# Kernel tuning notes

Measured on AMD Instinct MI355X. Metric: run time of the kernel, lower is better.

Reference implementation:

```python
import jax, jax.numpy as jnp
import numpy as np

V, F, H, P, C = 50000, 300, 256, 128, 10   # vocab, emb dim, n_hid, n_penultimate, n_class
B, S, N = 128, 16, 64                      # docs, sentences/doc, word nodes/sentence (last = master)
G, T = B * S, B * S * N                    # sentence graphs, total word nodes
EPS = 1e-5


def _mp(h, adj, w1, b1, w2, b2):
    # MessagePassing: neighborhood aggregation (block-diag spmm) + 2-layer ReLU MLP
    m = jnp.einsum('gij,gjf->gif', adj, h)
    return jax.nn.relu(jax.nn.relu(m @ w1 + b1) @ w2 + b2)


def _att(h, w, b, v, use_master):
    # Attention readout: alpha = softmax(relu(hW+b)v) over nodes, weighted sum;
    # with master node, last node is split off and concatenated to the pooled vector.
    if use_master:
        t, h = h[:, -1, :], h[:, :-1, :]
    logits = jnp.einsum('gnh,h->gn', jax.nn.relu(h @ w + b), v)
    alpha = jax.nn.softmax(logits, axis=1)
    pooled = jnp.einsum('gn,gnh->gh', alpha, h)
    return jnp.concatenate([pooled, t], axis=1) if use_master else pooled


def setup_inputs():
    key = jax.random.key(0)
    ks = iter(jax.random.split(key, 40))
    def nrm(shape, s=0.05):
        return jax.random.normal(next(ks), shape, jnp.float32) * s
    x = jax.random.randint(next(ks), (T,), 0, V)
    adj = jax.random.uniform(next(ks), (G, N, N), jnp.float32)
    adj = adj / jnp.sum(adj, -1, keepdims=True)         # row-normalized word-graph blocks
    adj_s = jax.random.uniform(next(ks), (B, S, S), jnp.float32)
    adj_s = adj_s / jnp.sum(adj_s, -1, keepdims=True)   # sentence-graph blocks (unused in sentence_att branch)
    return dict(
        x=x, adj=adj, adj_s=adj_s, shape0=N, shape1=S,
        emb=nrm((V, F), 0.1),
        mp0_w1=nrm((F, H)), mp0_b1=jnp.zeros((H,)), mp0_w2=nrm((H, H)), mp0_b2=jnp.zeros((H,)),
        mp1_w1=nrm((H, H)), mp1_b1=jnp.zeros((H,)), mp1_w2=nrm((H, H)), mp1_b2=jnp.zeros((H,)),
        att0_w=nrm((H, H)), att0_b=jnp.zeros((H,)), att0_v=nrm((H,)),
        att1_w=nrm((H, H)), att1_b=jnp.zeros((H,)), att1_v=nrm((H,)),
        bn_gamma=jnp.ones((4 * H,)), bn_beta=jnp.zeros((4 * H,)),
        fc1_w=nrm((4 * H, H)), fc1_b=jnp.zeros((H,)),
        satt_w=nrm((H, H)), satt_b=jnp.zeros((H,)), satt_v=nrm((H,)),
        fc2_w=nrm((H, P)), fc2_b=jnp.zeros((P,)),
        fc3_w=nrm((P, C)), fc3_b=jnp.zeros((C,)),
    )


def reference(x, adj, adj_s, shape0, shape1, emb,
              mp0_w1, mp0_b1, mp0_w2, mp0_b2,
              mp1_w1, mp1_b1, mp1_w2, mp1_b2,
              att0_w, att0_b, att0_v, att1_w, att1_b, att1_v,
              bn_gamma, bn_beta, fc1_w, fc1_b,
              satt_w, satt_b, satt_v, fc2_w, fc2_b, fc3_w, fc3_b):
    h = emb[x].reshape(-1, shape0, emb.shape[1])        # [G, N, F] (dropout is identity at eval)
    reps = []
    for (w1, b1, w2, b2, aw, ab, av) in (
            (mp0_w1, mp0_b1, mp0_w2, mp0_b2, att0_w, att0_b, att0_v),
            (mp1_w1, mp1_b1, mp1_w2, mp1_b2, att1_w, att1_b, att1_v)):
        h = _mp(h, adj, w1, b1, w2, b2)                  # [G, N, H]
        reps.append(_att(h, aw, ab, av, True))           # [G, 2H]
    z = jnp.concatenate(reps, axis=1)                    # [G, 2*n_mp*H] = [G, 4H]
    mu, var = jnp.mean(z, 0), jnp.var(z, 0)              # BatchNorm1d (batch statistics)
    z = (z - mu) / jnp.sqrt(var + EPS) * bn_gamma + bn_beta
    z = jax.nn.relu(z @ fc1_w + fc1_b)                   # [G, H]
    z = z.reshape(-1, shape1, z.shape[1])                # [B, S, H]
    z = _att(z, satt_w, satt_b, satt_v, False)           # sentence attention -> [B, H]
    z = jax.nn.relu(z @ fc2_w + fc2_b)                   # [B, P]
    z = z @ fc3_w + fc3_b                                # [B, C]
    return jax.nn.log_softmax(z, axis=1)
```

## Files before the change

### kernel.cpp

```cpp
#include <hip/hip_runtime.h>
#include <math.h>


typedef unsigned short u16;
typedef __attribute__((ext_vector_type(8))) short bf16x8;
typedef __attribute__((ext_vector_type(4))) float f32x4;

__device__ __forceinline__ float b2f(u16 v){ return __uint_as_float(((unsigned)v)<<16); }
__device__ __forceinline__ u16 f2b(float f){
    unsigned u = __float_as_uint(f);
    return (u16)((u + 0x7FFFu + ((u>>16)&1u)) >> 16);
}
__device__ __forceinline__ ushort4 pack4(float a,float b,float c,float d){
    ushort4 o; o.x=f2b(a); o.y=f2b(b); o.z=f2b(c); o.w=f2b(d); return o;
}

#define SCOL_OFF 32768
__device__ __forceinline__ int srow_b(int nd, int f){
    return (nd*512 + f*2) ^ ((nd&7)<<4);
}
__device__ __forceinline__ int scol_b(int f, int nd){
    return SCOL_OFF + ((f*128 + nd*2) ^ ((f&7)<<4));
}
__device__ __forceinline__ int wfrag_off(int ni){
    return ((ni>>1)<<10) + ((ni&1)<<9);
}

__global__ __attribute__((amdgpu_flat_work_group_size(512,512),
                          amdgpu_waves_per_eu(1,2)))
void mega_k(
    const int* __restrict__ x, const u16* __restrict__ adjb,
    const u16* __restrict__ eprime,
    const u16* __restrict__ wb_w2a, const u16* __restrict__ wb_awa,
    const u16* __restrict__ wb_w1b, const u16* __restrict__ wb_w2b,
    const u16* __restrict__ wb_awb,
    const float* __restrict__ b1a, const float* __restrict__ b2a,
    const float* __restrict__ aba, const float* __restrict__ ava,
    const float* __restrict__ b1b, const float* __restrict__ b2b,
    const float* __restrict__ abb, const float* __restrict__ avb,
    u16* __restrict__ zb)
{
    __shared__ __align__(16) char sm[131072];
    const int tid = threadIdx.x;
    const int w = tid>>6, l = tid&63, lgp = l>>4, ll = l&15;
    const int q = w>>2, w4 = w&3, slab = w4*64;
    const long g = (long)blockIdx.x*2 + q;
    char* smq = sm + q*65536;
    const f32x4 zero4 = {0.f,0.f,0.f,0.f};

    {
        const int r2 = tid >> 3;
        const int fc = (tid & 7) * 32;
        #pragma unroll
        for (int q2=0; q2<2; ++q2){
            const u16* ep = eprime + (long)x[((long)blockIdx.x*2+q2)*64 + r2]*256 + fc;
            char* smr = sm + q2*65536;
            uint4 qa = *(const uint4*)(ep);
            uint4 qb = *(const uint4*)(ep + 8);
            uint4 qc = *(const uint4*)(ep + 16);
            uint4 qd = *(const uint4*)(ep + 24);
            #pragma unroll
            for (int qi=0; qi<4; ++qi){
                uint4 v = (qi==0)?qa:(qi==1)?qb:(qi==2)?qc:qd;
                unsigned xw[4] = {v.x, v.y, v.z, v.w};
                #pragma unroll
                for (int wi=0; wi<4; ++wi){
                    unsigned u = xw[wi];
                    int f0 = fc + qi*8 + wi*2;
                    *(u16*)(smr + scol_b(f0,   r2)) = (u16)(u & 0xffffu);
                    *(u16*)(smr + scol_b(f0+1, r2)) = (u16)(u >> 16);
                }
            }
        }
        __syncthreads();
    }

    const u16* adjg = adjb + g*4096;

    #pragma unroll 1
    for (int layer=0; layer<2; ++layer){
        const u16* wb_w2 = layer ? wb_w2b : wb_w2a;
        const u16* wb_aw = layer ? wb_awb : wb_awa;
        const float* b1  = layer ? b1b : b1a;
        const float* b2  = layer ? b2b : b2a;
        const float* ab  = layer ? abb : aba;
        const float* av  = layer ? avb : ava;
        const int zoff   = layer ? 512 : 0;

        {
            f32x4 acc[4][4];
            #pragma unroll
            for (int i=0;i<4;++i){
                #pragma unroll
                for (int j=0;j<4;++j) acc[i][j] = zero4;
            }
            #pragma unroll
            for (int t=0;t<2;++t){
                const int k0 = t*32 + lgp*8;
                bf16x8 a[4], b[4];
                #pragma unroll
                for (int mi=0;mi<4;++mi)
                    a[mi] = *(const bf16x8*)(smq + scol_b(slab + mi*16 + ll, k0));
                #pragma unroll
                for (int ni=0;ni<4;++ni)
                    b[ni] = *(const bf16x8*)(adjg + (ni*16+ll)*64 + k0);
                #pragma unroll
                for (int mi=0;mi<4;++mi){
                    #pragma unroll
                    for (int ni=0;ni<4;++ni)
                        acc[mi][ni] = __builtin_amdgcn_mfma_f32_16x16x32_bf16(a[mi], b[ni], acc[mi][ni],0,0,0);
                }
            }
            #pragma unroll
            for (int mi=0;mi<4;++mi){
                int f0 = slab + mi*16 + lgp*4;
                float4 bi = *(const float4*)(b1 + f0);
                #pragma unroll
                for (int ni=0;ni<4;++ni){
                    int nd = ni*16 + ll;
                    f32x4 v = acc[mi][ni];
                    *(ushort4*)(smq + srow_b(nd, f0)) = pack4(
                        fmaxf(v[0]+bi.x,0.f), fmaxf(v[1]+bi.y,0.f),
                        fmaxf(v[2]+bi.z,0.f), fmaxf(v[3]+bi.w,0.f));
                }
            }
            __syncthreads();
        }

        {
            f32x4 acc[4][4];
            #pragma unroll
            for (int i=0;i<4;++i){
                #pragma unroll
                for (int j=0;j<4;++j) acc[i][j] = zero4;
            }
            const u16* chw = wb_w2 + ((w4*2)<<10) + ll*32 + lgp*8;
            #pragma unroll
            for (int t=0;t<8;++t){
                const u16* ct = chw + t*8192;
                const int k0 = t*32 + lgp*8;
                bf16x8 cw0 = *(const bf16x8*)(ct + wfrag_off(0));
                bf16x8 cw1 = *(const bf16x8*)(ct + wfrag_off(1));
                bf16x8 cw2 = *(const bf16x8*)(ct + wfrag_off(2));
                bf16x8 cw3 = *(const bf16x8*)(ct + wfrag_off(3));
                bf16x8 b[4];
                #pragma unroll
                for (int ni=0;ni<4;++ni) b[ni] = *(const bf16x8*)(smq + srow_b(ni*16+ll, k0));
                #pragma unroll
                for (int ni=0;ni<4;++ni){
                    acc[0][ni] = __builtin_amdgcn_mfma_f32_16x16x32_bf16(cw0, b[ni], acc[0][ni],0,0,0);
                    acc[1][ni] = __builtin_amdgcn_mfma_f32_16x16x32_bf16(cw1, b[ni], acc[1][ni],0,0,0);
                    acc[2][ni] = __builtin_amdgcn_mfma_f32_16x16x32_bf16(cw2, b[ni], acc[2][ni],0,0,0);
                    acc[3][ni] = __builtin_amdgcn_mfma_f32_16x16x32_bf16(cw3, b[ni], acc[3][ni],0,0,0);
                }
            }
            __syncthreads();
            #pragma unroll
            for (int mi=0;mi<4;++mi){
                int f0 = slab + mi*16 + lgp*4;
                float4 bi = *(const float4*)(b2 + f0);
                #pragma unroll
                for (int ni=0;ni<4;++ni){
                    int nd = ni*16 + ll;
                    f32x4 v = acc[mi][ni];
                    *(ushort4*)(smq + srow_b(nd, f0)) = pack4(
                        fmaxf(v[0]+bi.x,0.f), fmaxf(v[1]+bi.y,0.f),
                        fmaxf(v[2]+bi.z,0.f), fmaxf(v[3]+bi.w,0.f));
                }
            }
            __syncthreads();
        }

        {
            f32x4 acc[4][4];
            #pragma unroll
            for (int i=0;i<4;++i){
                #pragma unroll
                for (int j=0;j<4;++j) acc[i][j] = zero4;
            }
            const u16* chw = wb_aw + ((w4*2)<<10) + ll*32 + lgp*8;
            #pragma unroll
            for (int t=0;t<8;++t){
                const u16* ct = chw + t*8192;
                const int k0 = t*32 + lgp*8;
                bf16x8 cw0 = *(const bf16x8*)(ct + wfrag_off(0));
                bf16x8 cw1 = *(const bf16x8*)(ct + wfrag_off(1));
                bf16x8 cw2 = *(const bf16x8*)(ct + wfrag_off(2));
                bf16x8 cw3 = *(const bf16x8*)(ct + wfrag_off(3));
                bf16x8 a[4];
                #pragma unroll
                for (int mi=0;mi<4;++mi) a[mi] = *(const bf16x8*)(smq + srow_b(mi*16+ll, k0));
                #pragma unroll
                for (int mi=0;mi<4;++mi){
                    acc[mi][0] = __builtin_amdgcn_mfma_f32_16x16x32_bf16(a[mi], cw0, acc[mi][0],0,0,0);
                    acc[mi][1] = __builtin_amdgcn_mfma_f32_16x16x32_bf16(a[mi], cw1, acc[mi][1],0,0,0);
                    acc[mi][2] = __builtin_amdgcn_mfma_f32_16x16x32_bf16(a[mi], cw2, acc[mi][2],0,0,0);
                    acc[mi][3] = __builtin_amdgcn_mfma_f32_16x16x32_bf16(a[mi], cw3, acc[mi][3],0,0,0);
                }
            }
            float abv[4], avv[4];
            #pragma unroll
            for (int ni=0;ni<4;++ni){
                int c = slab + ni*16 + ll;
                abv[ni] = ab[c]; avv[ni] = av[c];
            }
            float lgt[4][4];
            #pragma unroll
            for (int mi=0;mi<4;++mi){
                #pragma unroll
                for (int r=0;r<4;++r) lgt[mi][r] = 0.f;
            }
            #pragma unroll
            for (int mi=0;mi<4;++mi){
                #pragma unroll
                for (int ni=0;ni<4;++ni){
                    f32x4 v = acc[mi][ni];
                    #pragma unroll
                    for (int r=0;r<4;++r) lgt[mi][r] += fmaxf(v[r]+abv[ni],0.f)*avv[ni];
                }
            }
            #pragma unroll
            for (int mi=0;mi<4;++mi){
                #pragma unroll
                for (int r=0;r<4;++r){
                    float vv = lgt[mi][r];
                    vv += __shfl_xor(vv,1,64); vv += __shfl_xor(vv,2,64);
                    vv += __shfl_xor(vv,4,64); vv += __shfl_xor(vv,8,64);
                    lgt[mi][r] = vv;
                }
            }
            float* red = (float*)(smq + SCOL_OFF);
            if (ll == 0){
                #pragma unroll
                for (int mi=0;mi<4;++mi){
                    #pragma unroll
                    for (int r=0;r<4;++r){
                        int node = mi*16 + lgp*4 + r;
                        red[w4*64 + node] = lgt[mi][r];
                    }
                }
            }
            __syncthreads();
            if (tid < 128){
                int qs = tid >> 6, t64 = tid & 63;
                const float* rq = (const float*)(sm + qs*65536 + SCOL_OFF);
                float lv = rq[t64] + rq[64+t64] + rq[128+t64] + rq[192+t64];
                float v = (t64 < 63) ? lv : -INFINITY;
                float m = v;
                #pragma unroll
                for (int off=32; off; off>>=1) m = fmaxf(m, __shfl_xor(m, off, 64));
                float e = (t64 < 63) ? expf(v - m) : 0.f;
                float s = e;
                #pragma unroll
                for (int off=32; off; off>>=1) s += __shfl_xor(s, off, 64);
                *(float*)(sm + qs*65536 + SCOL_OFF + 1024 + t64*4) = e / s;
            }
            __syncthreads();
            {
                int qs = tid >> 8, c = tid & 255;
                char* smr = sm + qs*65536;
                const float* alpha = (const float*)(smr + SCOL_OFF + 1024);
                float pool = 0.f;
                for (int r=0;r<63;++r)
                    pool += alpha[r]*b2f(*(const u16*)(smr + srow_b(r,c)));
                long zb0 = ((long)blockIdx.x*2 + qs)*1024 + zoff;
                zb[zb0 + c]       = f2b(pool);
                zb[zb0 + 256 + c] = *(const u16*)(smr + srow_b(63,c));
            }
            __syncthreads();
        }

        if (layer == 0){
            f32x4 acc[4][4];
            #pragma unroll
            for (int i=0;i<4;++i){
                #pragma unroll
                for (int j=0;j<4;++j) acc[i][j] = zero4;
            }
            const u16* chw = wb_w1b + ((w4*2)<<10) + ll*32 + lgp*8;
            #pragma unroll
            for (int t=0;t<8;++t){
                const u16* ct = chw + t*8192;
                const int k0 = t*32 + lgp*8;
                bf16x8 cw0 = *(const bf16x8*)(ct + wfrag_off(0));
                bf16x8 cw1 = *(const bf16x8*)(ct + wfrag_off(1));
                bf16x8 cw2 = *(const bf16x8*)(ct + wfrag_off(2));
                bf16x8 cw3 = *(const bf16x8*)(ct + wfrag_off(3));
                bf16x8 a[4];
                #pragma unroll
                for (int mi=0;mi<4;++mi) a[mi] = *(const bf16x8*)(smq + srow_b(mi*16+ll, k0));
                #pragma unroll
                for (int mi=0;mi<4;++mi){
                    acc[mi][0] = __builtin_amdgcn_mfma_f32_16x16x32_bf16(a[mi], cw0, acc[mi][0],0,0,0);
                    acc[mi][1] = __builtin_amdgcn_mfma_f32_16x16x32_bf16(a[mi], cw1, acc[mi][1],0,0,0);
                    acc[mi][2] = __builtin_amdgcn_mfma_f32_16x16x32_bf16(a[mi], cw2, acc[mi][2],0,0,0);
                    acc[mi][3] = __builtin_amdgcn_mfma_f32_16x16x32_bf16(a[mi], cw3, acc[mi][3],0,0,0);
                }
            }
            __syncthreads();
            #pragma unroll
            for (int mi=0;mi<4;++mi){
                #pragma unroll
                for (int ni=0;ni<4;++ni){
                    int fo = slab + ni*16 + ll, nd0 = mi*16 + lgp*4;
                    f32x4 v = acc[mi][ni];
                    *(ushort4*)(smq + scol_b(fo,nd0)) = pack4(v[0],v[1],v[2],v[3]);
                }
            }
            __syncthreads();
        }
    }
}

__global__ __launch_bounds__(256) void eprime_k(
    const float* __restrict__ emb, const u16* __restrict__ blob,
    u16* __restrict__ eprime)
{
    __shared__ __align__(16) char sm[4096];
    const int h = blockIdx.x, m0 = blockIdx.y * 32;
    const int tid = threadIdx.x;
    const int w = tid>>6, l = tid&63, lgp = l>>4, ll = l&15;
    const f32x4 zero4 = {0.f,0.f,0.f,0.f};
    const int slab = h*4 + w;

    const int r  = tid >> 3;
    const int kc = (tid & 7) * 4;
    int rowg = m0 + r; if (rowg > 49999) rowg = 49999;
    const long arow = (long)rowg * 300;
    const int wbyte = (r*64 + (tid&7)*8) ^ ((r&7)<<4);

    float4 pv = (kc + 4 <= 300) ? *(const float4*)(emb + arow + kc)
                                : make_float4(0.f,0.f,0.f,0.f);
    const u16* chw = blob + (slab<<10) + ll*32 + lgp*8;
    bf16x8 w0 = *(const bf16x8*)(chw);
    bf16x8 w1 = *(const bf16x8*)(chw + 512);

    f32x4 acc[2][2];
    acc[0][0]=zero4; acc[0][1]=zero4; acc[1][0]=zero4; acc[1][1]=zero4;

    #pragma unroll
    for (int t=0;t<10;++t){
        float4 cur = pv;
        bf16x8 cw0 = w0, cw1 = w1;
        if (t < 9){
            int kn = (t+1)*32 + kc;
            pv = (kn + 4 <= 300) ? *(const float4*)(emb + arow + kn)
                                 : make_float4(0.f,0.f,0.f,0.f);
            const u16* nx = chw + (t+1)*8192;
            w0 = *(const bf16x8*)(nx);
            w1 = *(const bf16x8*)(nx + 512);
        }
        *(ushort4*)(sm + (t&1)*2048 + wbyte) = pack4(cur.x,cur.y,cur.z,cur.w);
        __syncthreads();
        const char* eb = sm + (t&1)*2048;
        bf16x8 a0, a1;
        {
            int row = ll;
            a0 = *(const bf16x8*)(eb + ((row*64 + lgp*16) ^ ((row&7)<<4)));
            row = 16 + ll;
            a1 = *(const bf16x8*)(eb + ((row*64 + lgp*16) ^ ((row&7)<<4)));
        }
        acc[0][0] = __builtin_amdgcn_mfma_f32_16x16x32_bf16(a0, cw0, acc[0][0],0,0,0);
        acc[0][1] = __builtin_amdgcn_mfma_f32_16x16x32_bf16(a0, cw1, acc[0][1],0,0,0);
        acc[1][0] = __builtin_amdgcn_mfma_f32_16x16x32_bf16(a1, cw0, acc[1][0],0,0,0);
        acc[1][1] = __builtin_amdgcn_mfma_f32_16x16x32_bf16(a1, cw1, acc[1][1],0,0,0);
        __syncthreads();
    }
    #pragma unroll
    for (int mi=0;mi<2;++mi){
        #pragma unroll
        for (int ni=0;ni<2;++ni){
            int col = h*128 + w*32 + ni*16 + ll;
            f32x4 v = acc[mi][ni];
            #pragma unroll
            for (int rr=0;rr<4;++rr){
                int row = m0 + mi*16 + lgp*4 + rr;
                if (row < 50000) eprime[(long)row*256 + col] = f2b(v[rr]);
            }
        }
    }
}

__global__ __launch_bounds__(256) void conv_all_k(
    const float* __restrict__ w1a, const float* __restrict__ w2a,
    const float* __restrict__ awa, const float* __restrict__ w1b,
    const float* __restrict__ w2b, const float* __restrict__ awb,
    u16* __restrict__ dst_base)
{
    long idx = (long)blockIdx.x*256 + threadIdx.x;
    if (idx >= 81920L + 5L*65536L) return;
    const float* src; u16* dst; int Ksrc; long rem;
    if (idx < 81920L){ src = w1a; dst = dst_base; Ksrc = 300; rem = idx; }
    else {
        long j = (idx - 81920L) / 65536L, r2 = (idx - 81920L) % 65536L;
        src = (j==0)?w2a:(j==1)?awa:(j==2)?w1b:(j==3)?w2b:awb;
        dst = dst_base + 81920L + j*65536L; Ksrc = 256; rem = r2;
    }
    int k = (int)(rem >> 8), n = (int)(rem & 255);
    float v = (k < Ksrc) ? src[k*256 + n] : 0.f;
    int t = k>>5, kk = k&31;
    dst[((t*8 + (n>>5))<<10) + (n&31)*32 + kk] = f2b(v);
}

__global__ __launch_bounds__(256) void adjconv_k(
    const float* __restrict__ adj, u16* __restrict__ adjb)
{
    long i = (long)blockIdx.x*256 + threadIdx.x;
    if (i < 2048L*4096L) adjb[i] = f2b(adj[i]);
}

__global__ __launch_bounds__(256) void bnstats_k(
    const u16* __restrict__ zb, const float* __restrict__ gamma,
    const float* __restrict__ beta,
    float* __restrict__ scale, float* __restrict__ shift)
{
    const int tid = threadIdx.x;
    const int cl = tid & 3, ph = tid >> 2;
    const int c = blockIdx.x * 4 + cl;
    double s = 0.0, s2 = 0.0;
    #pragma unroll 8
    for (int r = ph; r < 2048; r += 64) {
        float v = b2f(zb[(long)r * 1024 + c]);
        s += v; s2 += (double)v * v;
    }
    __shared__ double ss[256], ss2[256];
    ss[tid] = s; ss2[tid] = s2;
    __syncthreads();
    for (int off = 128; off >= 4; off >>= 1){
        if (tid < off){ ss[tid] += ss[tid+off]; ss2[tid] += ss2[tid+off]; }
        __syncthreads();
    }
    if (tid < 4){
        int cc = blockIdx.x * 4 + tid;
        double mu = ss[tid] / 2048.0;
        double var = ss2[tid] / 2048.0 - mu * mu;
        float inv = (float)(1.0 / sqrt(var + 1e-5));
        float sc = gamma[cc] * inv;
        scale[cc] = sc;
        shift[cc] = beta[cc] - (float)mu * sc;
    }
}

__global__ __launch_bounds__(256) void wconv_fc1_k(
    const float* __restrict__ fw, const float* __restrict__ scale,
    u16* __restrict__ dst)
{
    int lin = blockIdx.x*256 + threadIdx.x;
    int c = lin >> 10, t = c >> 3, s = c & 7;
    int nl = (lin >> 5) & 31, kk = lin & 31;
    int n = s*32 + nl, k = t*32 + kk;
    dst[lin] = f2b(fw[k*256 + n] * scale[k]);
}

__global__ __launch_bounds__(256) void fusefc1_k(
    const float* __restrict__ fw, const float* __restrict__ shift,
    const float* __restrict__ fb, float* __restrict__ biasp)
{
    const int n = blockIdx.x, tid = threadIdx.x;
    float p = 0.f;
    #pragma unroll
    for (int i=0;i<4;++i){
        int k = tid + i*256;
        p += shift[k] * fw[k*256 + n];
    }
    __shared__ float red[256];
    red[tid] = p;
    __syncthreads();
    for (int off=128; off; off>>=1){
        if (tid < off) red[tid] += red[tid+off];
        __syncthreads();
    }
    if (tid == 0) biasp[n] = fb[n] + red[0];
}

__global__ __launch_bounds__(256) void fc1_mfma_k(
    const u16* __restrict__ zb, const u16* __restrict__ blob,
    const float* __restrict__ biasp, float* __restrict__ z2)
{
    __shared__ __align__(16) char sm[4096];
    const int h = blockIdx.x, m0 = blockIdx.y * 32;
    const int tid = threadIdx.x;
    const int w = tid>>6, l = tid&63, lgp = l>>4, ll = l&15;
    const f32x4 zero4 = {0.f,0.f,0.f,0.f};
    const int slab = h*4 + w;

    const int r  = tid >> 3;
    const int kc = (tid & 7) * 4;
    const long arow = (long)(m0 + r) * 1024;
    const int wbyte = (r*64 + (tid&7)*8) ^ ((r&7)<<4);

    ushort4 pv = *(const ushort4*)(zb + arow + kc);
    const u16* chw = blob + (slab<<10) + ll*32 + lgp*8;
    bf16x8 w0 = *(const bf16x8*)(chw);
    bf16x8 w1 = *(const bf16x8*)(chw + 512);

    f32x4 acc[2][2];
    acc[0][0]=zero4; acc[0][1]=zero4; acc[1][0]=zero4; acc[1][1]=zero4;

    #pragma unroll 4
    for (int t=0;t<32;++t){
        ushort4 cur = pv;
        bf16x8 cw0 = w0, cw1 = w1;
        if (t < 31){
            pv = *(const ushort4*)(zb + arow + (t+1)*32 + kc);
            const u16* nx = chw + (t+1)*8192;
            w0 = *(const bf16x8*)(nx);
            w1 = *(const bf16x8*)(nx + 512);
        }
        *(ushort4*)(sm + (t&1)*2048 + wbyte) = cur;
        __syncthreads();
        const char* eb = sm + (t&1)*2048;
        bf16x8 a0, a1;
        {
            int row = ll;
            a0 = *(const bf16x8*)(eb + ((row*64 + lgp*16) ^ ((row&7)<<4)));
            row = 16 + ll;
            a1 = *(const bf16x8*)(eb + ((row*64 + lgp*16) ^ ((row&7)<<4)));
        }
        acc[0][0] = __builtin_amdgcn_mfma_f32_16x16x32_bf16(a0, cw0, acc[0][0],0,0,0);
        acc[0][1] = __builtin_amdgcn_mfma_f32_16x16x32_bf16(a0, cw1, acc[0][1],0,0,0);
        acc[1][0] = __builtin_amdgcn_mfma_f32_16x16x32_bf16(a1, cw0, acc[1][0],0,0,0);
        acc[1][1] = __builtin_amdgcn_mfma_f32_16x16x32_bf16(a1, cw1, acc[1][1],0,0,0);
        __syncthreads();
    }
    #pragma unroll
    for (int mi=0;mi<2;++mi){
        #pragma unroll
        for (int ni=0;ni<2;++ni){
            int col = h*128 + w*32 + ni*16 + ll;
            float bv = biasp[col];
            f32x4 v = acc[mi][ni];
            #pragma unroll
            for (int rr=0;rr<4;++rr){
                int row = m0 + mi*16 + lgp*4 + rr;
                z2[(long)row*256 + col] = fmaxf(v[rr] + bv, 0.f);
            }
        }
    }
}

__global__ __launch_bounds__(256) void sattfinal_k(
    const float* __restrict__ z2, const float* __restrict__ sw,
    const float* __restrict__ sb, const float* __restrict__ sv,
    const float* __restrict__ w2, const float* __restrict__ b2,
    const float* __restrict__ w3, const float* __restrict__ b3,
    float* __restrict__ out)
{
    const int b = blockIdx.x;
    const int tid = threadIdx.x;
    __shared__ float zs[16][256];
    for (int idx = tid; idx < 16 * 256; idx += 256) {
        int r = idx >> 8, c = idx & 255;
        zs[r][c] = z2[((long)b * 16 + r) * 256 + c];
    }
    __syncthreads();

    float acc[16] = {};
    for (int k = 0; k < 256; ++k) {
        float w = sw[k * 256 + tid];
        #pragma unroll
        for (int r = 0; r < 16; ++r) acc[r] += zs[r][k] * w;
    }
    const float sbv = sb[tid], svv = sv[tid];

    __shared__ float red[16][4];
    __shared__ float logit_s[16], alpha_s[16];
    const int warp = tid >> 6, lane = tid & 63;
    #pragma unroll
    for (int r = 0; r < 16; ++r) {
        float u = fmaxf(acc[r] + sbv, 0.f);
        float lv = u * svv;
        #pragma unroll
        for (int off = 32; off; off >>= 1) lv += __shfl_down(lv, off, 64);
        if (lane == 0) red[r][warp] = lv;
    }
    __syncthreads();
    if (tid < 16) logit_s[tid] = red[tid][0] + red[tid][1] + red[tid][2] + red[tid][3];
    __syncthreads();
    if (tid < 16) {
        float m = -INFINITY;
        #pragma unroll
        for (int i = 0; i < 16; ++i) m = fmaxf(m, logit_s[i]);
        float ssum = 0.f;
        #pragma unroll
        for (int i = 0; i < 16; ++i) ssum += expf(logit_s[i] - m);
        alpha_s[tid] = expf(logit_s[tid] - m) / ssum;
    }
    __syncthreads();
    float pacc = 0.f;
    #pragma unroll
    for (int r = 0; r < 16; ++r) pacc += alpha_s[r] * zs[r][tid];

    __shared__ float ps[256], z3s[128], z4s[10];
    ps[tid] = pacc;
    __syncthreads();
    if (tid < 128){
        float a2 = b2[tid];
        for (int k = 0; k < 256; ++k) a2 += ps[k] * w2[k * 128 + tid];
        z3s[tid] = fmaxf(a2, 0.f);
    }
    __syncthreads();
    if (tid < 10){
        float a3 = b3[tid];
        for (int k = 0; k < 128; ++k) a3 += z3s[k] * w3[k * 10 + tid];
        z4s[tid] = a3;
    }
    __syncthreads();
    if (tid < 10){
        float m = z4s[0];
        #pragma unroll
        for (int i = 1; i < 10; ++i) m = fmaxf(m, z4s[i]);
        float s = 0.f;
        #pragma unroll
        for (int i = 0; i < 10; ++i) s += expf(z4s[i] - m);
        out[b * 10 + tid] = z4s[tid] - m - logf(s);
    }
}

extern "C" void kernel_launch(void* const* d_in, const int* in_sizes, int n_in,
                              void* d_out, int out_size, void* d_ws, size_t ws_size,
                              hipStream_t stream)
{
    const int*   x      = (const int*)d_in[0];
    const float* adj    = (const float*)d_in[1];
    const float* emb    = (const float*)d_in[5];
    const float* mp0_w1 = (const float*)d_in[6];
    const float* mp0_b1 = (const float*)d_in[7];
    const float* mp0_w2 = (const float*)d_in[8];
    const float* mp0_b2 = (const float*)d_in[9];
    const float* mp1_w1 = (const float*)d_in[10];
    const float* mp1_b1 = (const float*)d_in[11];
    const float* mp1_w2 = (const float*)d_in[12];
    const float* mp1_b2 = (const float*)d_in[13];
    const float* att0_w = (const float*)d_in[14];
    const float* att0_b = (const float*)d_in[15];
    const float* att0_v = (const float*)d_in[16];
    const float* att1_w = (const float*)d_in[17];
    const float* att1_b = (const float*)d_in[18];
    const float* att1_v = (const float*)d_in[19];
    const float* bn_g   = (const float*)d_in[20];
    const float* bn_b   = (const float*)d_in[21];
    const float* fc1_w  = (const float*)d_in[22];
    const float* fc1_b  = (const float*)d_in[23];
    const float* satt_w = (const float*)d_in[24];
    const float* satt_b = (const float*)d_in[25];
    const float* satt_v = (const float*)d_in[26];
    const float* fc2_w  = (const float*)d_in[27];
    const float* fc2_b  = (const float*)d_in[28];
    const float* fc3_w  = (const float*)d_in[29];
    const float* fc3_b  = (const float*)d_in[30];
    float* out = (float*)d_out;

    float* ws = (float*)d_ws;
    float* z2      = ws;
    float* scale   = z2 + 2048L * 256;
    float* shiftv  = scale + 1024;
    float* biasp   = shiftv + 1024;
    u16*   wbase   = (u16*)(biasp + 256);
    u16* wb_w1a  = wbase;
    u16* wb_w2a  = wb_w1a + 81920;
    u16* wb_awa  = wb_w2a + 65536;
    u16* wb_w1b  = wb_awa + 65536;
    u16* wb_w2b  = wb_w1b + 65536;
    u16* wb_awb  = wb_w2b + 65536;
    u16* adjb    = wb_awb + 65536;
    u16* zb      = adjb + 2048L*4096;
    u16* fc1blob = zb + 2048L*1024;
    u16* eprime  = fc1blob + 262144;

    conv_all_k<<<dim3(1600), dim3(256), 0, stream>>>(
        mp0_w1, mp0_w2, att0_w, mp1_w1, mp1_w2, att1_w, wbase);
    adjconv_k<<<dim3(32768), dim3(256), 0, stream>>>(adj, adjb);
    eprime_k<<<dim3(2, 1563), dim3(256), 0, stream>>>(emb, wb_w1a, eprime);

    mega_k<<<dim3(1024), dim3(512), 0, stream>>>(
        x, adjb, eprime,
        wb_w2a, wb_awa, wb_w1b, wb_w2b, wb_awb,
        mp0_b1, mp0_b2, att0_b, att0_v,
        mp1_b1, mp1_b2, att1_b, att1_v, zb);

    bnstats_k<<<dim3(256), dim3(256), 0, stream>>>(zb, bn_g, bn_b, scale, shiftv);
    wconv_fc1_k<<<dim3(1024), dim3(256), 0, stream>>>(fc1_w, scale, fc1blob);
    fusefc1_k<<<dim3(256), dim3(256), 0, stream>>>(fc1_w, shiftv, fc1_b, biasp);
    fc1_mfma_k<<<dim3(2, 64), dim3(256), 0, stream>>>(zb, fc1blob, biasp, z2);
    sattfinal_k<<<dim3(128), dim3(256), 0, stream>>>(z2, satt_w, satt_b, satt_v,
        fc2_w, fc2_b, fc3_w, fc3_b, out);
}
```

Baseline: 311.4 us.

## Ping-pong shared-memory buffers and split GEMM tiles into halves to cut registers

Each per-graph 64KB shared region now holds two 32KB buffers that alternate between stages (pA/pB swapped per layer), so GEMM outputs go to the other buffer. This removes the mid-stage __syncthreads that guarded in-place overwrites. Each wave's 4x4 accumulator tile is also processed as two 4x2 or 2x4 halves to shrink live accumulator registers, at the cost of reloading operand fragments (weights or adj) twice. Launch bounds change to __launch_bounds__(512,1).

```diff
diff --git a/kernel.cpp b/kernel.cpp
--- a/kernel.cpp
+++ b/kernel.cpp
@@ -15,20 +15,17 @@
     ushort4 o; o.x=f2b(a); o.y=f2b(b); o.z=f2b(c); o.w=f2b(d); return o;
 }
 
-#define SCOL_OFF 32768
-__device__ __forceinline__ int srow_b(int nd, int f){
+__device__ __forceinline__ int srow_rb(int nd, int f){
     return (nd*512 + f*2) ^ ((nd&7)<<4);
 }
-__device__ __forceinline__ int scol_b(int f, int nd){
-    return SCOL_OFF + ((f*128 + nd*2) ^ ((f&7)<<4));
+__device__ __forceinline__ int scol_rb(int f, int nd){
+    return (f*128 + nd*2) ^ ((f&7)<<4);
 }
 __device__ __forceinline__ int wfrag_off(int ni){
     return ((ni>>1)<<10) + ((ni&1)<<9);
 }
 
-__global__ __attribute__((amdgpu_flat_work_group_size(512,512),
-                          amdgpu_waves_per_eu(1,2)))
-void mega_k(
+__global__ __launch_bounds__(512, 1) void mega_k(
     const int* __restrict__ x, const u16* __restrict__ adjb,
     const u16* __restrict__ eprime,
     const u16* __restrict__ wb_w2a, const u16* __restrict__ wb_awa,
@@ -54,7 +51,7 @@
         #pragma unroll
         for (int q2=0; q2<2; ++q2){
             const u16* ep = eprime + (long)x[((long)blockIdx.x*2+q2)*64 + r2]*256 + fc;
-            char* smr = sm + q2*65536;
+            char* smr = sm + q2*65536 + 32768;
             uint4 qa = *(const uint4*)(ep);
             uint4 qb = *(const uint4*)(ep + 8);
             uint4 qc = *(const uint4*)(ep + 16);
@@ -67,8 +64,8 @@
                 for (int wi=0; wi<4; ++wi){
                     unsigned u = xw[wi];
                     int f0 = fc + qi*8 + wi*2;
-                    *(u16*)(smr + scol_b(f0,   r2)) = (u16)(u & 0xffffu);
-                    *(u16*)(smr + scol_b(f0+1, r2)) = (u16)(u >> 16);
+                    *(u16*)(smr + scol_rb(f0,   r2)) = (u16)(u & 0xffffu);
+                    *(u16*)(smr + scol_rb(f0+1, r2)) = (u16)(u >> 16);
                 }
             }
         }
@@ -86,29 +83,28 @@
         const float* ab  = layer ? abb : aba;
         const float* av  = layer ? avb : ava;
         const int zoff   = layer ? 512 : 0;
-
-        {
-            f32x4 acc[4][4];
-            #pragma unroll
-            for (int i=0;i<4;++i){
-                #pragma unroll
-                for (int j=0;j<4;++j) acc[i][j] = zero4;
-            }
+        const int pA = layer ? 0 : 32768;
+        const int pB = layer ? 32768 : 0;
+
+        #pragma unroll
+        for (int nh=0; nh<2; ++nh){
+            f32x4 acc[4][2];
+            #pragma unroll
+            for (int i=0;i<4;++i){ acc[i][0] = zero4; acc[i][1] = zero4; }
             #pragma unroll
             for (int t=0;t<2;++t){
                 const int k0 = t*32 + lgp*8;
-                bf16x8 a[4], b[4];
+                bf16x8 a[4], b[2];
                 #pragma unroll
                 for (int mi=0;mi<4;++mi)
-                    a[mi] = *(const bf16x8*)(smq + scol_b(slab + mi*16 + ll, k0));
-                #pragma unroll
-                for (int ni=0;ni<4;++ni)
-                    b[ni] = *(const bf16x8*)(adjg + (ni*16+ll)*64 + k0);
+                    a[mi] = *(const bf16x8*)(smq + pA + scol_rb(slab + mi*16 + ll, k0));
+                #pragma unroll
+                for (int ni=0;ni<2;++ni)
+                    b[ni] = *(const bf16x8*)(adjg + ((nh*2+ni)*16+ll)*64 + k0);
                 #pragma unroll
                 for (int mi=0;mi<4;++mi){
-                    #pragma unroll
-                    for (int ni=0;ni<4;++ni)
-                        acc[mi][ni] = __builtin_amdgcn_mfma_f32_16x16x32_bf16(a[mi], b[ni], acc[mi][ni],0,0,0);
+                    acc[mi][0] = __builtin_amdgcn_mfma_f32_16x16x32_bf16(a[mi], b[0], acc[mi][0],0,0,0);
+                    acc[mi][1] = __builtin_amdgcn_mfma_f32_16x16x32_bf16(a[mi], b[1], acc[mi][1],0,0,0);
                 }
             }
             #pragma unroll
@@ -116,24 +112,22 @@
                 int f0 = slab + mi*16 + lgp*4;
                 float4 bi = *(const float4*)(b1 + f0);
                 #pragma unroll
-                for (int ni=0;ni<4;++ni){
-                    int nd = ni*16 + ll;
+                for (int ni=0;ni<2;++ni){
+                    int nd = (nh*2+ni)*16 + ll;
                     f32x4 v = acc[mi][ni];
-                    *(ushort4*)(smq + srow_b(nd, f0)) = pack4(
+                    *(ushort4*)(smq + pB + srow_rb(nd, f0)) = pack4(
                         fmaxf(v[0]+bi.x,0.f), fmaxf(v[1]+bi.y,0.f),
                         fmaxf(v[2]+bi.z,0.f), fmaxf(v[3]+bi.w,0.f));
                 }
             }
-            __syncthreads();
-        }
-
-        {
-            f32x4 acc[4][4];
-            #pragma unroll
-            for (int i=0;i<4;++i){
-                #pragma unroll
-                for (int j=0;j<4;++j) acc[i][j] = zero4;
-            }
+        }
+        __syncthreads();
+
+        #pragma unroll
+        for (int nh=0; nh<2; ++nh){
+            f32x4 acc[4][2];
+            #pragma unroll
+            for (int i=0;i<4;++i){ acc[i][0] = zero4; acc[i][1] = zero4; }
             const u16* chw = wb_w2 + ((w4*2)<<10) + ll*32 + lgp*8;
             #pragma unroll
             for (int t=0;t<8;++t){
@@ -143,107 +137,108 @@
                 bf16x8 cw1 = *(const bf16x8*)(ct + wfrag_off(1));
                 bf16x8 cw2 = *(const bf16x8*)(ct + wfrag_off(2));
                 bf16x8 cw3 = *(const bf16x8*)(ct + wfrag_off(3));
-                bf16x8 b[4];
-                #pragma unroll
-                for (int ni=0;ni<4;++ni) b[ni] = *(const bf16x8*)(smq + srow_b(ni*16+ll, k0));
-                #pragma unroll
-                for (int ni=0;ni<4;++ni){
+                bf16x8 b[2];
+                #pragma unroll
+                for (int ni=0;ni<2;++ni)
+                    b[ni] = *(const bf16x8*)(smq + pB + srow_rb((nh*2+ni)*16+ll, k0));
+                #pragma unroll
+                for (int ni=0;ni<2;++ni){
                     acc[0][ni] = __builtin_amdgcn_mfma_f32_16x16x32_bf16(cw0, b[ni], acc[0][ni],0,0,0);
                     acc[1][ni] = __builtin_amdgcn_mfma_f32_16x16x32_bf16(cw1, b[ni], acc[1][ni],0,0,0);
                     acc[2][ni] = __builtin_amdgcn_mfma_f32_16x16x32_bf16(cw2, b[ni], acc[2][ni],0,0,0);
                     acc[3][ni] = __builtin_amdgcn_mfma_f32_16x16x32_bf16(cw3, b[ni], acc[3][ni],0,0,0);
                 }
             }
-            __syncthreads();
             #pragma unroll
             for (int mi=0;mi<4;++mi){
                 int f0 = slab + mi*16 + lgp*4;
                 float4 bi = *(const float4*)(b2 + f0);
                 #pragma unroll
-                for (int ni=0;ni<4;++ni){
-                    int nd = ni*16 + ll;
+                for (int ni=0;ni<2;++ni){
+                    int nd = (nh*2+ni)*16 + ll;
                     f32x4 v = acc[mi][ni];
-                    *(ushort4*)(smq + srow_b(nd, f0)) = pack4(
+                    *(ushort4*)(smq + pA + srow_rb(nd, f0)) = pack4(
                         fmaxf(v[0]+bi.x,0.f), fmaxf(v[1]+bi.y,0.f),
                         fmaxf(v[2]+bi.z,0.f), fmaxf(v[3]+bi.w,0.f));
                 }
             }
-            __syncthreads();
-        }
+        }
+        __syncthreads();
 
         {
-            f32x4 acc[4][4];
-            #pragma unroll
-            for (int i=0;i<4;++i){
-                #pragma unroll
-                for (int j=0;j<4;++j) acc[i][j] = zero4;
-            }
-            const u16* chw = wb_aw + ((w4*2)<<10) + ll*32 + lgp*8;
-            #pragma unroll
-            for (int t=0;t<8;++t){
-                const u16* ct = chw + t*8192;
-                const int k0 = t*32 + lgp*8;
-                bf16x8 cw0 = *(const bf16x8*)(ct + wfrag_off(0));
-                bf16x8 cw1 = *(const bf16x8*)(ct + wfrag_off(1));
-                bf16x8 cw2 = *(const bf16x8*)(ct + wfrag_off(2));
-                bf16x8 cw3 = *(const bf16x8*)(ct + wfrag_off(3));
-                bf16x8 a[4];
-                #pragma unroll
-                for (int mi=0;mi<4;++mi) a[mi] = *(const bf16x8*)(smq + srow_b(mi*16+ll, k0));
-                #pragma unroll
-                for (int mi=0;mi<4;++mi){
-                    acc[mi][0] = __builtin_amdgcn_mfma_f32_16x16x32_bf16(a[mi], cw0, acc[mi][0],0,0,0);
-                    acc[mi][1] = __builtin_amdgcn_mfma_f32_16x16x32_bf16(a[mi], cw1, acc[mi][1],0,0,0);
-                    acc[mi][2] = __builtin_amdgcn_mfma_f32_16x16x32_bf16(a[mi], cw2, acc[mi][2],0,0,0);
-                    acc[mi][3] = __builtin_amdgcn_mfma_f32_16x16x32_bf16(a[mi], cw3, acc[mi][3],0,0,0);
-                }
-            }
             float abv[4], avv[4];
             #pragma unroll
             for (int ni=0;ni<4;++ni){
                 int c = slab + ni*16 + ll;
                 abv[ni] = ab[c]; avv[ni] = av[c];
             }
-            float lgt[4][4];
-            #pragma unroll
-            for (int mi=0;mi<4;++mi){
-                #pragma unroll
-                for (int r=0;r<4;++r) lgt[mi][r] = 0.f;
-            }
-            #pragma unroll
-            for (int mi=0;mi<4;++mi){
-                #pragma unroll
-                for (int ni=0;ni<4;++ni){
-                    f32x4 v = acc[mi][ni];
-                    #pragma unroll
-                    for (int r=0;r<4;++r) lgt[mi][r] += fmaxf(v[r]+abv[ni],0.f)*avv[ni];
-                }
-            }
-            #pragma unroll
-            for (int mi=0;mi<4;++mi){
-                #pragma unroll
-                for (int r=0;r<4;++r){
-                    float vv = lgt[mi][r];
-                    vv += __shfl_xor(vv,1,64); vv += __shfl_xor(vv,2,64);
-                    vv += __shfl_xor(vv,4,64); vv += __shfl_xor(vv,8,64);
-                    lgt[mi][r] = vv;
-                }
-            }
-            float* red = (float*)(smq + SCOL_OFF);
-            if (ll == 0){
-                #pragma unroll
-                for (int mi=0;mi<4;++mi){
+            float* red = (float*)(smq + pB);
+            #pragma unroll
+            for (int mh=0; mh<2; ++mh){
+                f32x4 acc[2][4];
+                #pragma unroll
+                for (int j=0;j<4;++j){ acc[0][j] = zero4; acc[1][j] = zero4; }
+                const u16* chw = wb_aw + ((w4*2)<<10) + ll*32 + lgp*8;
+                #pragma unroll
+                for (int t=0;t<8;++t){
+                    const u16* ct = chw + t*8192;
+                    const int k0 = t*32 + lgp*8;
+                    bf16x8 cw0 = *(const bf16x8*)(ct + wfrag_off(0));
+                    bf16x8 cw1 = *(const bf16x8*)(ct + wfrag_off(1));
+                    bf16x8 cw2 = *(const bf16x8*)(ct + wfrag_off(2));
+                    bf16x8 cw3 = *(const bf16x8*)(ct + wfrag_off(3));
+                    bf16x8 a[2];
+                    #pragma unroll
+                    for (int mi=0;mi<2;++mi)
+                        a[mi] = *(const bf16x8*)(smq + pA + srow_rb((mh*2+mi)*16+ll, k0));
+                    #pragma unroll
+                    for (int mi=0;mi<2;++mi){
+                        acc[mi][0] = __builtin_amdgcn_mfma_f32_16x16x32_bf16(a[mi], cw0, acc[mi][0],0,0,0);
+                        acc[mi][1] = __builtin_amdgcn_mfma_f32_16x16x32_bf16(a[mi], cw1, acc[mi][1],0,0,0);
+                        acc[mi][2] = __builtin_amdgcn_mfma_f32_16x16x32_bf16(a[mi], cw2, acc[mi][2],0,0,0);
+                        acc[mi][3] = __builtin_amdgcn_mfma_f32_16x16x32_bf16(a[mi], cw3, acc[mi][3],0,0,0);
+                    }
+                }
+                float lgt[2][4];
+                #pragma unroll
+                for (int mi=0;mi<2;++mi){
+                    #pragma unroll
+                    for (int r=0;r<4;++r) lgt[mi][r] = 0.f;
+                }
+                #pragma unroll
+                for (int mi=0;mi<2;++mi){
+                    #pragma unroll
+                    for (int ni=0;ni<4;++ni){
+                        f32x4 v = acc[mi][ni];
+                        #pragma unroll
+                        for (int r=0;r<4;++r) lgt[mi][r] += fmaxf(v[r]+abv[ni],0.f)*avv[ni];
+                    }
+                }
+                #pragma unroll
+                for (int mi=0;mi<2;++mi){
                     #pragma unroll
                     for (int r=0;r<4;++r){
-                        int node = mi*16 + lgp*4 + r;
-                        red[w4*64 + node] = lgt[mi][r];
+                        float vv = lgt[mi][r];
+                        vv += __shfl_xor(vv,1,64); vv += __shfl_xor(vv,2,64);
+                        vv += __shfl_xor(vv,4,64); vv += __shfl_xor(vv,8,64);
+                        lgt[mi][r] = vv;
+                    }
+                }
+                if (ll == 0){
+                    #pragma unroll
+                    for (int mi=0;mi<2;++mi){
+                        #pragma unroll
+                        for (int r=0;r<4;++r){
+                            int node = (mh*2+mi)*16 + lgp*4 + r;
+                            red[w4*64 + node] = lgt[mi][r];
+                        }
                     }
                 }
             }
             __syncthreads();
             if (tid < 128){
                 int qs = tid >> 6, t64 = tid & 63;
-                const float* rq = (const float*)(sm + qs*65536 + SCOL_OFF);
+                const float* rq = (const float*)(sm + qs*65536 + pB);
                 float lv = rq[t64] + rq[64+t64] + rq[128+t64] + rq[192+t64];
                 float v = (t64 < 63) ? lv : -INFINITY;
                 float m = v;
@@ -253,58 +248,54 @@
                 float s = e;
                 #pragma unroll
                 for (int off=32; off; off>>=1) s += __shfl_xor(s, off, 64);
-                *(float*)(sm + qs*65536 + SCOL_OFF + 1024 + t64*4) = e / s;
+                *(float*)(sm + qs*65536 + pB + 1024 + t64*4) = e / s;
             }
             __syncthreads();
             {
                 int qs = tid >> 8, c = tid & 255;
                 char* smr = sm + qs*65536;
-                const float* alpha = (const float*)(smr + SCOL_OFF + 1024);
+                const float* alpha = (const float*)(smr + pB + 1024);
                 float pool = 0.f;
                 for (int r=0;r<63;++r)
-                    pool += alpha[r]*b2f(*(const u16*)(smr + srow_b(r,c)));
+                    pool += alpha[r]*b2f(*(const u16*)(smr + pA + srow_rb(r,c)));
                 long zb0 = ((long)blockIdx.x*2 + qs)*1024 + zoff;
                 zb[zb0 + c]       = f2b(pool);
-                zb[zb0 + 256 + c] = *(const u16*)(smr + srow_b(63,c));
+                zb[zb0 + 256 + c] = *(const u16*)(smr + pA + srow_rb(63,c));
             }
             __syncthreads();
         }
 
         if (layer == 0){
-            f32x4 acc[4][4];
-            #pragma unroll
-            for (int i=0;i<4;++i){
-                #pragma unroll
-                for (int j=0;j<4;++j) acc[i][j] = zero4;
-            }
-            const u16* chw = wb_w1b + ((w4*2)<<10) + ll*32 + lgp*8;
-            #pragma unroll
-            for (int t=0;t<8;++t){
-                const u16* ct = chw + t*8192;
-                const int k0 = t*32 + lgp*8;
-                bf16x8 cw0 = *(const bf16x8*)(ct + wfrag_off(0));
-                bf16x8 cw1 = *(const bf16x8*)(ct + wfrag_off(1));
-                bf16x8 cw2 = *(const bf16x8*)(ct + wfrag_off(2));
-                bf16x8 cw3 = *(const bf16x8*)(ct + wfrag_off(3));
-                bf16x8 a[4];
-                #pragma unroll
-                for (int mi=0;mi<4;++mi) a[mi] = *(const bf16x8*)(smq + srow_b(mi*16+ll, k0));
+            #pragma unroll
+            for (int nh=0; nh<2; ++nh){
+                f32x4 acc[4][2];
+                #pragma unroll
+                for (int i=0;i<4;++i){ acc[i][0] = zero4; acc[i][1] = zero4; }
+                const u16* chw = wb_w1b + ((w4*2)<<10) + ll*32 + lgp*8;
+                #pragma unroll
+                for (int t=0;t<8;++t){
+                    const u16* ct = chw + t*8192;
+                    const int k0 = t*32 + lgp*8;
+                    bf16x8 cwA = *(const bf16x8*)(ct + wfrag_off(nh*2+0));
+                    bf16x8 cwB = *(const bf16x8*)(ct + wfrag_off(nh*2+1));
+                    bf16x8 a[4];
+                    #pragma unroll
+                    for (int mi=0;mi<4;++mi)
+                        a[mi] = *(const bf16x8*)(smq + pA + srow_rb(mi*16+ll, k0));
+                    #pragma unroll
+                    for (int mi=0;mi<4;++mi){
+                        acc[mi][0] = __builtin_amdgcn_mfma_f32_16x16x32_bf16(a[mi], cwA, acc[mi][0],0,0,0);
+                        acc[mi][1] = __builtin_amdgcn_mfma_f32_16x16x32_bf16(a[mi], cwB, acc[mi][1],0,0,0);
+                    }
+                }
                 #pragma unroll
                 for (int mi=0;mi<4;++mi){
-                    acc[mi][0] = __builtin_amdgcn_mfma_f32_16x16x32_bf16(a[mi], cw0, acc[mi][0],0,0,0);
-                    acc[mi][1] = __builtin_amdgcn_mfma_f32_16x16x32_bf16(a[mi], cw1, acc[mi][1],0,0,0);
-                    acc[mi][2] = __builtin_amdgcn_mfma_f32_16x16x32_bf16(a[mi], cw2, acc[mi][2],0,0,0);
-                    acc[mi][3] = __builtin_amdgcn_mfma_f32_16x16x32_bf16(a[mi], cw3, acc[mi][3],0,0,0);
-                }
-            }
-            __syncthreads();
-            #pragma unroll
-            for (int mi=0;mi<4;++mi){
-                #pragma unroll
-                for (int ni=0;ni<4;++ni){
-                    int fo = slab + ni*16 + ll, nd0 = mi*16 + lgp*4;
-                    f32x4 v = acc[mi][ni];
-                    *(ushort4*)(smq + scol_b(fo,nd0)) = pack4(v[0],v[1],v[2],v[3]);
+                    #pragma unroll
+                    for (int ni=0;ni<2;++ni){
+                        int fo = slab + (nh*2+ni)*16 + ll, nd0 = mi*16 + lgp*4;
+                        f32x4 v = acc[mi][ni];
+                        *(ushort4*)(smq + pB + scol_rb(fo,nd0)) = pack4(v[0],v[1],v[2],v[3]);
+                    }
                 }
             }
             __syncthreads();
```

Measured after the change: 392.6 us. +26.1%, slower.
